# Kernel optimization log

Hardware: AMD Instinct MI355X
Metric: run time of the kernel (lower is better)

Reference implementation:

```python
import jax, jax.numpy as jnp
import numpy as np
from jax import lax

NUM_HEADS = 8
EPS = 1e-12  # torch F.normalize default eps


def setup_inputs() -> dict:
    key = jax.random.key(0)
    ks = jax.random.split(key, 5)
    b, c, h, w = 8, 128, 128, 128
    return {
        "x_in": jax.random.normal(ks[0], (b, c, h, w), dtype=jnp.float32),
        "illu_fea": jax.random.normal(ks[1], (b, c, h, w), dtype=jnp.float32),
        "w_qkv": jax.random.normal(ks[2], (3 * c, c), dtype=jnp.float32) * 0.05,
        "w_dw": jax.random.normal(ks[3], (3 * c, 1, 3, 3), dtype=jnp.float32) * 0.2,
        "w_proj": jax.random.normal(ks[4], (c, c), dtype=jnp.float32) * 0.05,
        "temperature": jnp.ones((NUM_HEADS, 1, 1), dtype=jnp.float32),
    }


def _l2norm(t):
    # F.normalize(t, dim=-1, p=2): t / max(||t||_2, eps)
    n = jnp.sqrt(jnp.sum(t * t, axis=-1, keepdims=True))
    return t / jnp.maximum(n, EPS)


def reference(x_in, illu_fea, w_qkv, w_dw, w_proj, temperature):
    b, c, h, w = x_in.shape
    dh = c // NUM_HEADS
    # 1x1 conv (pointwise channel GEMM): [b,c,h,w] -> [b,3c,h,w]
    qkv = jnp.einsum("bchw,oc->bohw", x_in, w_qkv)
    # depthwise 3x3 conv, groups = 3c, SAME padding
    qkv = lax.conv_general_dilated(
        qkv, w_dw, window_strides=(1, 1), padding="SAME",
        dimension_numbers=("NCHW", "OIHW", "NCHW"),
        feature_group_count=3 * c,
    )
    q, k, v = jnp.split(qkv, 3, axis=1)
    # b (head dh) h w -> b head dh (h*w)
    rs = lambda t: t.reshape(b, NUM_HEADS, dh, h * w)
    q, k, v = rs(q), rs(k), rs(v)
    v = v * illu_fea.reshape(b, NUM_HEADS, dh, h * w)  # illumination gating
    q = _l2norm(q)
    k = _l2norm(k)
    # channel-wise attention: [b,head,dh,dh], contract over spatial N = h*w
    attn = jnp.einsum("bhcn,bhdn->bhcd", q, k) * temperature
    attn = jax.nn.softmax(attn, axis=-1)
    out = jnp.einsum("bhcd,bhdn->bhcn", attn, v).reshape(b, c, h, w)
    out = jnp.einsum("bchw,oc->bohw", out, w_proj)  # project_out 1x1 conv
    return out
```

## Files before the change

kernel.cpp:

```cpp
#include <hip/hip_runtime.h>
#include <hip/hip_bf16.h>

typedef __attribute__((ext_vector_type(8))) short bf16x8;
typedef __attribute__((ext_vector_type(4))) float f32x4;

__device__ __forceinline__ unsigned short f2b(float f) {
    unsigned int u = __builtin_bit_cast(unsigned int, f);
    u += 0x7FFFu + ((u >> 16) & 1u);
    return (unsigned short)(u >> 16);
}
__device__ __forceinline__ float b2f(unsigned short h) {
    unsigned int u = ((unsigned int)h) << 16;
    return __builtin_bit_cast(float, u);
}

#define OFFB_QKV1 0L
#define OFFB_SLOT2 100663296L
#define OFFB_WBF  201326592L
#define OFFB_G    201424896L
#define OFFB_NQK  201490432L
#define OFFB_CTB  201564160L

__global__ __launch_bounds__(256) void prep_w_zero(const float* __restrict__ w,
                                                   unsigned short* __restrict__ wbf,
                                                   float* __restrict__ Gz)
{
    if (blockIdx.x < 48) {
        int e = blockIdx.x * 256 + threadIdx.x;
        float4 v = *(const float4*)&w[e * 4];
        unsigned int p0 = (unsigned int)f2b(v.x) | ((unsigned int)f2b(v.y) << 16);
        unsigned int p1 = (unsigned int)f2b(v.z) | ((unsigned int)f2b(v.w) << 16);
        *(uint2*)&wbf[e * 4] = make_uint2(p0, p1);
    } else {
        for (int i = threadIdx.x; i < 18432; i += 256) Gz[i] = 0.f;
    }
}

__global__ __launch_bounds__(256) void transpose_cb(const float* __restrict__ in,
                                                    unsigned short* __restrict__ out)
{
    const int b  = blockIdx.z;
    const int c0 = blockIdx.y * 32;
    const int n0 = blockIdx.x * 64;
    __shared__ float s[32][65];
    const int tid = threadIdx.x;
    const float* ib = in + ((long)b * 128 + c0) * 16384 + n0;
#pragma unroll
    for (int i = 0; i < 2; ++i) {
        int e = tid + i * 256;
        int c = e >> 4, n4 = (e & 15) * 4;
        *(float4*)&s[c][n4] = *(const float4*)&ib[(long)c * 16384 + n4];
    }
    __syncthreads();
    const int n = tid >> 2, cg = (tid & 3) * 8;
    unsigned int p[4];
#pragma unroll
    for (int j = 0; j < 4; ++j)
        p[j] = (unsigned int)f2b(s[cg + 2*j][n]) | ((unsigned int)f2b(s[cg + 2*j + 1][n]) << 16);
    *(uint4*)&out[((long)b * 16384 + n0 + n) * 128 + c0 + cg] = make_uint4(p[0], p[1], p[2], p[3]);
}

__global__ __launch_bounds__(256) void mfma_gemm_k1(
    const unsigned short* __restrict__ A,
    const unsigned short* __restrict__ Bt, unsigned short* __restrict__ C)
{
    const int b  = blockIdx.z;
    const int m0 = blockIdx.y * 128;
    const int n0 = blockIdx.x * 128;
    const unsigned short* Ab = A + (long)m0 * 128;
    const unsigned short* Bb = Bt + ((long)b * 16384 + n0) * 128;

    __shared__ unsigned short As[128][136];
    __shared__ unsigned short Bs[128][136];

    const int tid = threadIdx.x;
#pragma unroll
    for (int i = 0; i < 8; ++i) {
        int ch = tid + i * 256;
        int row = ch >> 4, cg = (ch & 15) * 8;
        *(uint4*)&As[row][cg] = *(const uint4*)&Ab[row * 128 + cg];
        *(uint4*)&Bs[row][cg] = *(const uint4*)&Bb[row * 128 + cg];
    }
    __syncthreads();

    const int l  = tid & 63;
    const int w  = tid >> 6;
    const int mb = (w & 1) * 64, nb = (w >> 1) * 64;
    const int lr = l & 15, lg = l >> 4;

    f32x4 acc[4][4];
    const f32x4 zero = {0.f, 0.f, 0.f, 0.f};
#pragma unroll
    for (int mi = 0; mi < 4; ++mi)
#pragma unroll
        for (int ni = 0; ni < 4; ++ni) acc[mi][ni] = zero;

#pragma unroll
    for (int kk = 0; kk < 128; kk += 32) {
        bf16x8 af[4], bfr[4];
#pragma unroll
        for (int mi = 0; mi < 4; ++mi)
            af[mi] = *(const bf16x8*)&As[mb + mi * 16 + lr][kk + lg * 8];
#pragma unroll
        for (int ni = 0; ni < 4; ++ni)
            bfr[ni] = *(const bf16x8*)&Bs[nb + ni * 16 + lr][kk + lg * 8];
#pragma unroll
        for (int mi = 0; mi < 4; ++mi)
#pragma unroll
            for (int ni = 0; ni < 4; ++ni)
                acc[mi][ni] = __builtin_amdgcn_mfma_f32_16x16x32_bf16(
                    af[mi], bfr[ni], acc[mi][ni], 0, 0, 0);
    }

    __syncthreads();
    unsigned short* ct = &As[0][0];
#pragma unroll
    for (int mi = 0; mi < 4; ++mi)
#pragma unroll
        for (int ni = 0; ni < 4; ++ni)
#pragma unroll
            for (int r = 0; r < 4; ++r)
                ct[(mb + mi * 16 + lg * 4 + r) * 128 + nb + ni * 16 + lr] =
                    f2b(acc[mi][ni][r]);
    __syncthreads();
    unsigned short* Cg = C + ((long)b * 384 + m0) * 16384 + n0;
#pragma unroll
    for (int i = 0; i < 8; ++i) {
        int ch = tid + i * 256;
        int row = ch >> 4, cg = (ch & 15) * 8;
        *(uint4*)&Cg[(long)row * 16384 + cg] = *(const uint4*)&ct[row * 128 + cg];
    }
}

__global__ __launch_bounds__(256) void dw_qk_gram(
    const unsigned short* __restrict__ qkv1, const float* __restrict__ wdw,
    float* __restrict__ G, float* __restrict__ nqk)
{
    const int strip = blockIdx.x, hd = blockIdx.y, b = blockIdx.z;
    const int y0 = strip * 8;
    const int tid = threadIdx.x;
    const int l = tid & 63, w = tid >> 6;
    const int lr = l & 15, lg = l >> 4;

    __shared__ unsigned short st[10][130][18];
    __shared__ float sg[4][16][16];

    if (tid < 180) {
        int y = tid / 18, c = tid - y * 18;
        st[y][0][c] = 0; st[y][129][c] = 0;
    }

    const int sch = tid & 15;
    const int sxc = tid >> 4;

    bf16x8 af[8];
    f32x4 acc = {0.f, 0.f, 0.f, 0.f};
    float qn = 0.f, kn = 0.f;

    for (int op = 0; op < 2; ++op) {
        const int chbase = op * 128 + hd * 16;
        __syncthreads();
        const unsigned short* src = qkv1 + ((long)b * 384 + chbase + sch) * 16384;
#pragma unroll
        for (int y = 0; y < 10; ++y) {
            int yy = y0 + y - 1;
            uint4 v = make_uint4(0, 0, 0, 0);
            if (yy >= 0 && yy < 128) v = *(const uint4*)&src[yy * 128 + sxc * 8];
            unsigned short* d = &st[y][sxc * 8 + 1][sch];
            d[0]   = (unsigned short)(v.x);
            d[18]  = (unsigned short)(v.x >> 16);
            d[36]  = (unsigned short)(v.y);
            d[54]  = (unsigned short)(v.y >> 16);
            d[72]  = (unsigned short)(v.z);
            d[90]  = (unsigned short)(v.z >> 16);
            d[108] = (unsigned short)(v.w);
            d[126] = (unsigned short)(v.w >> 16);
        }
        __syncthreads();

        float wv[9];
#pragma unroll
        for (int j = 0; j < 9; ++j) wv[j] = wdw[(chbase + lr) * 9 + j];

#pragma unroll
        for (int j = 0; j < 8; ++j) {
            const int yb = 2 * w + (j >> 2);
            const int x0 = (j & 3) * 32 + lg * 8;
            float r0[10], r1[10], r2[10];
#pragma unroll
            for (int i = 0; i < 10; ++i) {
                r0[i] = b2f(st[yb][x0 + i][lr]);
                r1[i] = b2f(st[yb + 1][x0 + i][lr]);
                r2[i] = b2f(st[yb + 2][x0 + i][lr]);
            }
            bf16x8 fr;
            float nrm = 0.f;
#pragma unroll
            for (int i = 0; i < 8; ++i) {
                float a = 0.f;
                a = fmaf(wv[0], r0[i], a); a = fmaf(wv[1], r0[i+1], a); a = fmaf(wv[2], r0[i+2], a);
                a = fmaf(wv[3], r1[i], a); a = fmaf(wv[4], r1[i+1], a); a = fmaf(wv[5], r1[i+2], a);
                a = fmaf(wv[6], r2[i], a); a = fmaf(wv[7], r2[i+1], a); a = fmaf(wv[8], r2[i+2], a);
                unsigned short hh = f2b(a);
                fr[i] = (short)hh;
                float f = b2f(hh);
                nrm = fmaf(f, f, nrm);
            }
            if (op == 0) { af[j] = fr; qn += nrm; }
            else {
                kn += nrm;
                acc = __builtin_amdgcn_mfma_f32_16x16x32_bf16(af[j], fr, acc, 0, 0, 0);
            }
        }
    }

    qn += __shfl_xor(qn, 16); qn += __shfl_xor(qn, 32);
    kn += __shfl_xor(kn, 16); kn += __shfl_xor(kn, 32);
    if (l < 16) {
        atomicAdd(&nqk[b * 256 + hd * 16 + lr], qn);
        atomicAdd(&nqk[b * 256 + 128 + hd * 16 + lr], kn);
    }

#pragma unroll
    for (int r = 0; r < 4; ++r) sg[w][lg * 4 + r][lr] = acc[r];
    __syncthreads();
    const int row = tid >> 4, col = tid & 15;
    float v = sg[0][row][col] + sg[1][row][col] + sg[2][row][col] + sg[3][row][col];
    atomicAdd(&G[(((long)b * 8 + hd) * 16 + row) * 16 + col], v);
}

__global__ __launch_bounds__(256) void dw_v_gate(
    const unsigned short* __restrict__ qkv1, const float* __restrict__ wdw,
    const float* __restrict__ illu, unsigned short* __restrict__ Vg)
{
    const int b = blockIdx.z, c = blockIdx.y;
    const int ch = 256 + c;
    const int y0 = blockIdx.x * 16;
    const int tid = threadIdx.x;
    __shared__ float lds[18][136];
    const unsigned short* in = qkv1 + ((long)b * 384 + ch) * 16384;

    float wv[9];
#pragma unroll
    for (int j = 0; j < 9; ++j) wv[j] = wdw[ch * 9 + j];

#pragma unroll
    for (int i = 0; i < 2; ++i) {
        int chk = tid + i * 256;
        if (chk < 288) {
            int row = chk >> 4, xg = (chk & 15) * 8;
            int yy = y0 + row - 1;
            float f[8];
            if (yy >= 0 && yy < 128) {
                uint4 v = *(const uint4*)&in[yy * 128 + xg];
                unsigned int uu[4] = {v.x, v.y, v.z, v.w};
#pragma unroll
                for (int j = 0; j < 4; ++j) {
                    f[2*j]   = __builtin_bit_cast(float, uu[j] << 16);
                    f[2*j+1] = __builtin_bit_cast(float, uu[j] & 0xFFFF0000u);
                }
            } else {
#pragma unroll
                for (int j = 0; j < 8; ++j) f[j] = 0.f;
            }
            *(float4*)&lds[row][xg + 4] = make_float4(f[0], f[1], f[2], f[3]);
            *(float4*)&lds[row][xg + 8] = make_float4(f[4], f[5], f[6], f[7]);
        }
    }
    if (tid < 18) lds[tid][3] = 0.f;
    else if (tid < 50 && tid >= 32) lds[tid - 32][132] = 0.f;
    __syncthreads();

    const int x  = tid & 127;
    const int rt = (tid >> 7) * 8;
    float c0[10], c1[10], c2[10];
#pragma unroll
    for (int t = 0; t < 10; ++t) {
        c0[t] = lds[rt + t][x + 3];
        c1[t] = lds[rt + t][x + 4];
        c2[t] = lds[rt + t][x + 5];
    }
    const float* ib = illu + ((long)b * 128 + c) * 16384 + y0 * 128;
    unsigned short* ob = Vg + ((long)b * 128 + c) * 16384 + y0 * 128;
#pragma unroll
    for (int rr = 0; rr < 8; ++rr) {
        float a = 0.f;
        a = fmaf(wv[0], c0[rr],     a); a = fmaf(wv[1], c1[rr],     a); a = fmaf(wv[2], c2[rr],     a);
        a = fmaf(wv[3], c0[rr + 1], a); a = fmaf(wv[4], c1[rr + 1], a); a = fmaf(wv[5], c2[rr + 1], a);
        a = fmaf(wv[6], c0[rr + 2], a); a = fmaf(wv[7], c1[rr + 2], a); a = fmaf(wv[8], c2[rr + 2], a);
        int ry = rt + rr;
        ob[ry * 128 + x] = f2b(a * ib[ry * 128 + x]);
    }
}

__global__ __launch_bounds__(256) void softmax_compose(
    const float* __restrict__ G, const float* __restrict__ nqk,
    const float* __restrict__ temp, const float* __restrict__ wproj,
    unsigned short* __restrict__ CtBo)
{
    const int b = blockIdx.x;
    const int tid = threadIdx.x;
    __shared__ float sa[8][16][16];
    if (tid < 128) {
        const int hd = tid >> 4, r = tid & 15;
        const float tv = temp[hd];
        const float* g = G + ((long)(b * 8 + hd) * 16 + r) * 16;
        float mq = fmaxf(sqrtf(nqk[b * 256 + hd * 16 + r]), 1e-12f);
        float L[16];
        float mx = -1e30f;
#pragma unroll
        for (int d = 0; d < 16; ++d) {
            float mk = fmaxf(sqrtf(nqk[b * 256 + 128 + hd * 16 + d]), 1e-12f);
            L[d] = g[d] * tv / (mq * mk);
            mx = fmaxf(mx, L[d]);
        }
        float s = 0.f;
#pragma unroll
        for (int d = 0; d < 16; ++d) { L[d] = expf(L[d] - mx); s += L[d]; }
        float inv = 1.f / s;
#pragma unroll
        for (int d = 0; d < 16; ++d) sa[hd][r][d] = L[d] * inv;
    }
    __syncthreads();
#pragma unroll 1
    for (int e = tid; e < 16384; e += 256) {
        const int o = e >> 7, D = e & 127;
        const int hd2 = D >> 4, d = D & 15;
        const float* wr = wproj + o * 128 + hd2 * 16;
        float s = 0.f;
#pragma unroll
        for (int c2 = 0; c2 < 16; ++c2) s = fmaf(wr[c2], sa[hd2][c2][d], s);
        CtBo[((long)b * 128 + o) * 128 + D] = f2b(s);
    }
}

__global__ __launch_bounds__(256) void mfma_k6(
    const unsigned short* __restrict__ CtBo, const unsigned short* __restrict__ Vg,
    float* __restrict__ out)
{
    const int b  = blockIdx.y;
    const int n0 = blockIdx.x * 128;
    __shared__ unsigned short As[128][136];
    __shared__ unsigned short Bs[128][136];
    __shared__ float sfl[32][65];
    const int tid = threadIdx.x;

    const unsigned short* Ab = CtBo + (long)b * 16384;
#pragma unroll
    for (int i = 0; i < 8; ++i) {
        int ch = tid + i * 256;
        int row = ch >> 4, cg = (ch & 15) * 8;
        *(uint4*)&As[row][cg] = *(const uint4*)&Ab[row * 128 + cg];
    }

    const unsigned short* Vb = Vg + (long)b * 128 * 16384;
#pragma unroll 1
    for (int it = 0; it < 8; ++it) {
        const int c0 = (it & 3) * 32, nb0 = (it >> 2) * 64;
        {
            int c = tid >> 3, n8 = (tid & 7) * 8;
            uint4 v = *(const uint4*)&Vb[(long)(c0 + c) * 16384 + n0 + nb0 + n8];
            unsigned int uu[4] = {v.x, v.y, v.z, v.w};
#pragma unroll
            for (int j = 0; j < 4; ++j) {
                sfl[c][n8 + 2*j]     = __builtin_bit_cast(float, uu[j] << 16);
                sfl[c][n8 + 2*j + 1] = __builtin_bit_cast(float, uu[j] & 0xFFFF0000u);
            }
        }
        __syncthreads();
        {
            int n = tid >> 2, cg = (tid & 3) * 8;
            unsigned int p[4];
#pragma unroll
            for (int j = 0; j < 4; ++j)
                p[j] = (unsigned int)f2b(sfl[cg + 2*j][n]) | ((unsigned int)f2b(sfl[cg + 2*j + 1][n]) << 16);
            *(uint4*)&Bs[nb0 + n][c0 + cg] = make_uint4(p[0], p[1], p[2], p[3]);
        }
        __syncthreads();
    }

    const int l  = tid & 63;
    const int w  = tid >> 6;
    const int mb = (w & 1) * 64, nb = (w >> 1) * 64;
    const int lr = l & 15, lg = l >> 4;

    f32x4 acc[4][4];
    const f32x4 zero = {0.f, 0.f, 0.f, 0.f};
#pragma unroll
    for (int mi = 0; mi < 4; ++mi)
#pragma unroll
        for (int ni = 0; ni < 4; ++ni) acc[mi][ni] = zero;

#pragma unroll
    for (int kk = 0; kk < 128; kk += 32) {
        bf16x8 af[4], bfr[4];
#pragma unroll
        for (int mi = 0; mi < 4; ++mi)
            af[mi] = *(const bf16x8*)&As[mb + mi * 16 + lr][kk + lg * 8];
#pragma unroll
        for (int ni = 0; ni < 4; ++ni)
            bfr[ni] = *(const bf16x8*)&Bs[nb + ni * 16 + lr][kk + lg * 8];
#pragma unroll
        for (int mi = 0; mi < 4; ++mi)
#pragma unroll
            for (int ni = 0; ni < 4; ++ni)
                acc[mi][ni] = __builtin_amdgcn_mfma_f32_16x16x32_bf16(
                    af[mi], bfr[ni], acc[mi][ni], 0, 0, 0);
    }

    float* Cg = out + ((long)b * 128) * 16384 + n0;
#pragma unroll
    for (int mi = 0; mi < 4; ++mi)
#pragma unroll
        for (int ni = 0; ni < 4; ++ni)
#pragma unroll
            for (int r = 0; r < 4; ++r)
                Cg[(long)(mb + mi * 16 + lg * 4 + r) * 16384 + nb + ni * 16 + lr] =
                    acc[mi][ni][r];
}

extern "C" void kernel_launch(void* const* d_in, const int* in_sizes, int n_in,
                              void* d_out, int out_size, void* d_ws, size_t ws_size,
                              hipStream_t stream)
{
    const float* x     = (const float*)d_in[0];
    const float* illu  = (const float*)d_in[1];
    const float* wqkv  = (const float*)d_in[2];
    const float* wdw   = (const float*)d_in[3];
    const float* wproj = (const float*)d_in[4];
    const float* temp  = (const float*)d_in[5];
    float* out = (float*)d_out;
    char*  wsb = (char*)d_ws;

    unsigned short* qkv1 = (unsigned short*)(wsb + OFFB_QKV1);
    unsigned short* xT   = (unsigned short*)(wsb + OFFB_SLOT2);
    unsigned short* Vg   = (unsigned short*)(wsb + OFFB_SLOT2);
    unsigned short* wbf  = (unsigned short*)(wsb + OFFB_WBF);
    float* G    = (float*)(wsb + OFFB_G);
    float* nqk  = (float*)(wsb + OFFB_NQK);
    unsigned short* CtBo = (unsigned short*)(wsb + OFFB_CTB);

    hipLaunchKernelGGL(prep_w_zero, dim3(49), dim3(256), 0, stream, wqkv, wbf, G);
    hipLaunchKernelGGL(transpose_cb, dim3(256, 4, 8), dim3(256), 0, stream, x, xT);
    hipLaunchKernelGGL(mfma_gemm_k1, dim3(128, 3, 8), dim3(256), 0, stream,
                       wbf, xT, qkv1);
    hipLaunchKernelGGL(dw_v_gate, dim3(8, 128, 8), dim3(256), 0, stream,
                       qkv1, wdw, illu, Vg);
    hipLaunchKernelGGL(dw_qk_gram, dim3(16, 8, 8), dim3(256), 0, stream,
                       qkv1, wdw, G, nqk);
    hipLaunchKernelGGL(softmax_compose, dim3(8), dim3(256), 0, stream,
                       G, nqk, temp, wproj, CtBo);
    hipLaunchKernelGGL(mfma_k6, dim3(128, 8), dim3(256), 0, stream,
                       CtBo, Vg, out);
}
```

Before: 280.7 us.

## Fuse input transpose into QKV GEMM and switch dw_qk_gram LDS to channel-major

Merges the fp32-to-bf16 transpose kernel into the QKV pointwise GEMM. Each block now loads and transposes its x tile into LDS once and reuses it for all three 128-row weight tiles, which removes the xT round trip through global memory and one launch. It also changes the dw_qk_gram shared-memory staging from an interleaved [y][x][ch] layout to a channel-major layout with padded row strides, so stencil rows can be read with vector LDS loads instead of scalar ones. In exchange, the fused kernel launches a third as many blocks, uses more LDS per block, and runs its three output tiles serially, which may reduce occupancy and latency hiding.

```diff
diff --git a/kernel.cpp b/kernel.cpp
--- a/kernel.cpp
+++ b/kernel.cpp
@@ -36,102 +36,102 @@
     }
 }
 
-__global__ __launch_bounds__(256) void transpose_cb(const float* __restrict__ in,
-                                                    unsigned short* __restrict__ out)
-{
-    const int b  = blockIdx.z;
-    const int c0 = blockIdx.y * 32;
-    const int n0 = blockIdx.x * 64;
-    __shared__ float s[32][65];
+__global__ __launch_bounds__(256) void k1_fused(
+    const unsigned short* __restrict__ wbf,
+    const float* __restrict__ x,
+    unsigned short* __restrict__ qkv1)
+{
+    const int b = blockIdx.y, n0 = blockIdx.x * 128;
+    __shared__ unsigned short Bs[128][136];
+    __shared__ unsigned short As[128][136];
+    __shared__ float sfl[32][65];
     const int tid = threadIdx.x;
-    const float* ib = in + ((long)b * 128 + c0) * 16384 + n0;
-#pragma unroll
-    for (int i = 0; i < 2; ++i) {
-        int e = tid + i * 256;
-        int c = e >> 4, n4 = (e & 15) * 4;
-        *(float4*)&s[c][n4] = *(const float4*)&ib[(long)c * 16384 + n4];
-    }
-    __syncthreads();
-    const int n = tid >> 2, cg = (tid & 3) * 8;
-    unsigned int p[4];
-#pragma unroll
-    for (int j = 0; j < 4; ++j)
-        p[j] = (unsigned int)f2b(s[cg + 2*j][n]) | ((unsigned int)f2b(s[cg + 2*j + 1][n]) << 16);
-    *(uint4*)&out[((long)b * 16384 + n0 + n) * 128 + c0 + cg] = make_uint4(p[0], p[1], p[2], p[3]);
-}
-
-__global__ __launch_bounds__(256) void mfma_gemm_k1(
-    const unsigned short* __restrict__ A,
-    const unsigned short* __restrict__ Bt, unsigned short* __restrict__ C)
-{
-    const int b  = blockIdx.z;
-    const int m0 = blockIdx.y * 128;
-    const int n0 = blockIdx.x * 128;
-    const unsigned short* Ab = A + (long)m0 * 128;
-    const unsigned short* Bb = Bt + ((long)b * 16384 + n0) * 128;
-
-    __shared__ unsigned short As[128][136];
-    __shared__ unsigned short Bs[128][136];
-
-    const int tid = threadIdx.x;
-#pragma unroll
-    for (int i = 0; i < 8; ++i) {
-        int ch = tid + i * 256;
-        int row = ch >> 4, cg = (ch & 15) * 8;
-        *(uint4*)&As[row][cg] = *(const uint4*)&Ab[row * 128 + cg];
-        *(uint4*)&Bs[row][cg] = *(const uint4*)&Bb[row * 128 + cg];
-    }
-    __syncthreads();
+
+    const float* xb = x + (long)b * 128 * 16384 + n0;
+#pragma unroll 1
+    for (int it = 0; it < 8; ++it) {
+        const int c0 = (it & 3) * 32, nb0 = (it >> 2) * 64;
+        {
+            int c = tid >> 3, n8 = (tid & 7) * 8;
+            *(float4*)&sfl[c][n8]     = *(const float4*)&xb[(long)(c0 + c) * 16384 + nb0 + n8];
+            *(float4*)&sfl[c][n8 + 4] = *(const float4*)&xb[(long)(c0 + c) * 16384 + nb0 + n8 + 4];
+        }
+        __syncthreads();
+        {
+            int n = tid >> 2, cg = (tid & 3) * 8;
+            unsigned int p[4];
+#pragma unroll
+            for (int j = 0; j < 4; ++j)
+                p[j] = (unsigned int)f2b(sfl[cg + 2*j][n]) | ((unsigned int)f2b(sfl[cg + 2*j + 1][n]) << 16);
+            *(uint4*)&Bs[nb0 + n][c0 + cg] = make_uint4(p[0], p[1], p[2], p[3]);
+        }
+        __syncthreads();
+    }
 
     const int l  = tid & 63;
     const int w  = tid >> 6;
     const int mb = (w & 1) * 64, nb = (w >> 1) * 64;
     const int lr = l & 15, lg = l >> 4;
 
-    f32x4 acc[4][4];
-    const f32x4 zero = {0.f, 0.f, 0.f, 0.f};
-#pragma unroll
-    for (int mi = 0; mi < 4; ++mi)
-#pragma unroll
-        for (int ni = 0; ni < 4; ++ni) acc[mi][ni] = zero;
-
-#pragma unroll
-    for (int kk = 0; kk < 128; kk += 32) {
-        bf16x8 af[4], bfr[4];
+#pragma unroll 1
+    for (int mt = 0; mt < 3; ++mt) {
+        const unsigned short* Ab = wbf + (long)(mt * 128) * 128;
+#pragma unroll
+        for (int i = 0; i < 8; ++i) {
+            int ch = tid + i * 256;
+            int row = ch >> 4, cg = (ch & 15) * 8;
+            *(uint4*)&As[row][cg] = *(const uint4*)&Ab[row * 128 + cg];
+        }
+        __syncthreads();
+
+        f32x4 acc[4][4];
+        const f32x4 zero = {0.f, 0.f, 0.f, 0.f};
 #pragma unroll
         for (int mi = 0; mi < 4; ++mi)
-            af[mi] = *(const bf16x8*)&As[mb + mi * 16 + lr][kk + lg * 8];
-#pragma unroll
-        for (int ni = 0; ni < 4; ++ni)
-            bfr[ni] = *(const bf16x8*)&Bs[nb + ni * 16 + lr][kk + lg * 8];
+#pragma unroll
+            for (int ni = 0; ni < 4; ++ni) acc[mi][ni] = zero;
+
+#pragma unroll
+        for (int kk = 0; kk < 128; kk += 32) {
+            bf16x8 af[4], bfr[4];
+#pragma unroll
+            for (int mi = 0; mi < 4; ++mi)
+                af[mi] = *(const bf16x8*)&As[mb + mi * 16 + lr][kk + lg * 8];
+#pragma unroll
+            for (int ni = 0; ni < 4; ++ni)
+                bfr[ni] = *(const bf16x8*)&Bs[nb + ni * 16 + lr][kk + lg * 8];
+#pragma unroll
+            for (int mi = 0; mi < 4; ++mi)
+#pragma unroll
+                for (int ni = 0; ni < 4; ++ni)
+                    acc[mi][ni] = __builtin_amdgcn_mfma_f32_16x16x32_bf16(
+                        af[mi], bfr[ni], acc[mi][ni], 0, 0, 0);
+        }
+
+        __syncthreads();
+        unsigned short* ct = &As[0][0];
 #pragma unroll
         for (int mi = 0; mi < 4; ++mi)
 #pragma unroll
             for (int ni = 0; ni < 4; ++ni)
-                acc[mi][ni] = __builtin_amdgcn_mfma_f32_16x16x32_bf16(
-                    af[mi], bfr[ni], acc[mi][ni], 0, 0, 0);
-    }
-
-    __syncthreads();
-    unsigned short* ct = &As[0][0];
-#pragma unroll
-    for (int mi = 0; mi < 4; ++mi)
-#pragma unroll
-        for (int ni = 0; ni < 4; ++ni)
-#pragma unroll
-            for (int r = 0; r < 4; ++r)
-                ct[(mb + mi * 16 + lg * 4 + r) * 128 + nb + ni * 16 + lr] =
-                    f2b(acc[mi][ni][r]);
-    __syncthreads();
-    unsigned short* Cg = C + ((long)b * 384 + m0) * 16384 + n0;
-#pragma unroll
-    for (int i = 0; i < 8; ++i) {
-        int ch = tid + i * 256;
-        int row = ch >> 4, cg = (ch & 15) * 8;
-        *(uint4*)&Cg[(long)row * 16384 + cg] = *(const uint4*)&ct[row * 128 + cg];
-    }
-}
-
+#pragma unroll
+                for (int r = 0; r < 4; ++r)
+                    ct[(mb + mi * 16 + lg * 4 + r) * 128 + nb + ni * 16 + lr] =
+                        f2b(acc[mi][ni][r]);
+        __syncthreads();
+        unsigned short* Cg = qkv1 + ((long)b * 384 + mt * 128) * 16384 + n0;
+#pragma unroll
+        for (int i = 0; i < 8; ++i) {
+            int ch = tid + i * 256;
+            int row = ch >> 4, cg = (ch & 15) * 8;
+            *(uint4*)&Cg[(long)row * 16384 + cg] = *(const uint4*)&ct[row * 128 + cg];
+        }
+        __syncthreads();
+    }
+}
+
+#define CHS 1416
+#define YS  136
 __global__ __launch_bounds__(256) void dw_qk_gram(
     const unsigned short* __restrict__ qkv1, const float* __restrict__ wdw,
     float* __restrict__ G, float* __restrict__ nqk)
@@ -142,12 +142,13 @@
     const int l = tid & 63, w = tid >> 6;
     const int lr = l & 15, lg = l >> 4;
 
-    __shared__ unsigned short st[10][130][18];
+    __shared__ unsigned short st[16 * CHS];
     __shared__ float sg[4][16][16];
 
-    if (tid < 180) {
-        int y = tid / 18, c = tid - y * 18;
-        st[y][0][c] = 0; st[y][129][c] = 0;
+    if (tid < 160) {
+        int y = tid >> 4, c = tid & 15;
+        st[c * CHS + y * YS + 0]   = 0;
+        st[c * CHS + y * YS + 129] = 0;
     }
 
     const int sch = tid & 15;
@@ -161,20 +162,21 @@
         const int chbase = op * 128 + hd * 16;
         __syncthreads();
         const unsigned short* src = qkv1 + ((long)b * 384 + chbase + sch) * 16384;
+        unsigned short* dst = &st[sch * CHS + sxc * 8 + 1];
 #pragma unroll
         for (int y = 0; y < 10; ++y) {
             int yy = y0 + y - 1;
             uint4 v = make_uint4(0, 0, 0, 0);
             if (yy >= 0 && yy < 128) v = *(const uint4*)&src[yy * 128 + sxc * 8];
-            unsigned short* d = &st[y][sxc * 8 + 1][sch];
-            d[0]   = (unsigned short)(v.x);
-            d[18]  = (unsigned short)(v.x >> 16);
-            d[36]  = (unsigned short)(v.y);
-            d[54]  = (unsigned short)(v.y >> 16);
-            d[72]  = (unsigned short)(v.z);
-            d[90]  = (unsigned short)(v.z >> 16);
-            d[108] = (unsigned short)(v.w);
-            d[126] = (unsigned short)(v.w >> 16);
+            unsigned short* d = dst + y * YS;
+            d[0] = (unsigned short)(v.x);
+            d[1] = (unsigned short)(v.x >> 16);
+            d[2] = (unsigned short)(v.y);
+            d[3] = (unsigned short)(v.y >> 16);
+            d[4] = (unsigned short)(v.z);
+            d[5] = (unsigned short)(v.z >> 16);
+            d[6] = (unsigned short)(v.w);
+            d[7] = (unsigned short)(v.w >> 16);
         }
         __syncthreads();
 
@@ -186,12 +188,18 @@
         for (int j = 0; j < 8; ++j) {
             const int yb = 2 * w + (j >> 2);
             const int x0 = (j & 3) * 32 + lg * 8;
+            const unsigned short* rb = &st[lr * CHS + yb * YS + x0];
             float r0[10], r1[10], r2[10];
 #pragma unroll
-            for (int i = 0; i < 10; ++i) {
-                r0[i] = b2f(st[yb][x0 + i][lr]);
-                r1[i] = b2f(st[yb + 1][x0 + i][lr]);
-                r2[i] = b2f(st[yb + 2][x0 + i][lr]);
+            for (int rr = 0; rr < 3; ++rr) {
+                float* r = (rr == 0) ? r0 : (rr == 1) ? r1 : r2;
+                const unsigned short* p = rb + rr * YS;
+                bf16x8 a8 = *(const bf16x8*)p;
+                unsigned int t = *(const unsigned int*)(p + 8);
+#pragma unroll
+                for (int i = 0; i < 8; ++i) r[i] = b2f((unsigned short)a8[i]);
+                r[8] = b2f((unsigned short)(t & 0xFFFF));
+                r[9] = b2f((unsigned short)(t >> 16));
             }
             bf16x8 fr;
             float nrm = 0.f;
@@ -433,7 +441,6 @@
     char*  wsb = (char*)d_ws;
 
     unsigned short* qkv1 = (unsigned short*)(wsb + OFFB_QKV1);
-    unsigned short* xT   = (unsigned short*)(wsb + OFFB_SLOT2);
     unsigned short* Vg   = (unsigned short*)(wsb + OFFB_SLOT2);
     unsigned short* wbf  = (unsigned short*)(wsb + OFFB_WBF);
     float* G    = (float*)(wsb + OFFB_G);
@@ -441,9 +448,8 @@
     unsigned short* CtBo = (unsigned short*)(wsb + OFFB_CTB);
 
     hipLaunchKernelGGL(prep_w_zero, dim3(49), dim3(256), 0, stream, wqkv, wbf, G);
-    hipLaunchKernelGGL(transpose_cb, dim3(256, 4, 8), dim3(256), 0, stream, x, xT);
-    hipLaunchKernelGGL(mfma_gemm_k1, dim3(128, 3, 8), dim3(256), 0, stream,
-                       wbf, xT, qkv1);
+    hipLaunchKernelGGL(k1_fused, dim3(128, 8), dim3(256), 0, stream,
+                       wbf, x, qkv1);
     hipLaunchKernelGGL(dw_v_gate, dim3(8, 128, 8), dim3(256), 0, stream,
                        qkv1, wdw, illu, Vg);
     hipLaunchKernelGGL(dw_qk_gram, dim3(16, 8, 8), dim3(256), 0, stream,
```

Result: slower. 288.0 us (+2.6%).
